# Optimization experiments

Hardware: AMD Instinct MI355X
Metric: run time of the kernel (lower is better)

Reference implementation:

```python
import jax, jax.numpy as jnp
import numpy as np

B, N, C = 2, 65536, 256
H, D, S = 8, 64, 64  # heads, dim_head, slice_num
INNER = H * D


def setup_inputs() -> dict:
    key = jax.random.key(0)
    ks = jax.random.split(key, 8)
    scale_in = 1.0 / np.sqrt(C)
    scale_d = 1.0 / np.sqrt(D)
    return {
        "x": jax.random.normal(ks[0], (B, N, C), dtype=jnp.float32),
        "W_x": jax.random.uniform(ks[1], (C, INNER), jnp.float32, -scale_in, scale_in),
        "b_x": jax.random.uniform(ks[2], (INNER,), jnp.float32, -scale_in, scale_in),
        "W_fx": jax.random.uniform(ks[3], (C, INNER), jnp.float32, -scale_in, scale_in),
        "b_fx": jax.random.uniform(ks[4], (INNER,), jnp.float32, -scale_in, scale_in),
        "W_slice": jax.random.uniform(ks[5], (D, S), jnp.float32, -scale_d, scale_d),
        "b_slice": jax.random.uniform(ks[6], (S,), jnp.float32, -scale_d, scale_d),
        "temperature": jnp.full((1, H, 1, 1), 0.5, dtype=jnp.float32),
    }


def _split_heads(t):
    # (B, N, H*D) -> (B, H, N, D)
    return t.reshape(B, N, H, D).transpose(0, 2, 1, 3)


def reference(x, W_x, b_x, W_fx, b_fx, W_slice, b_slice, temperature):
    projected_x = _split_heads(x @ W_x + b_x)          # (B,H,N,D)
    fx = _split_heads(x @ W_fx + b_fx)                 # (B,H,N,D)
    slice_proj = projected_x @ W_slice + b_slice       # (B,H,N,S)
    temp = jnp.clip(temperature, 0.5, 5.0)
    slice_weights = jax.nn.softmax(slice_proj / temp, axis=-1)  # (B,H,N,S)
    slice_norm = slice_weights.sum(axis=2)             # (B,H,S)
    normed = slice_weights / (slice_norm[:, :, None, :] + 0.01)
    # weighted token aggregation: (B,H,S,D)
    slice_tokens = jnp.einsum("bhns,bhnd->bhsd", normed, fx)
    return slice_tokens
```

## Files before the change

### kernel.cpp

```cpp
#include <hip/hip_runtime.h>

typedef _Float16 f16;
typedef __attribute__((ext_vector_type(8))) _Float16 f16x8;
typedef __attribute__((ext_vector_type(4))) _Float16 f16x4;
typedef __attribute__((ext_vector_type(4))) float    f32x4;

#define MFMA(a,b,c) __builtin_amdgcn_mfma_f32_16x16x32_f16(a,b,c,0,0,0)

constexpr int Bc = 2, Nc = 65536, Cc = 256, Hc = 8;
constexpr int CHUNK = 512;
constexpr int LDX = 72;
constexpr int LDT = 136;


__device__ __forceinline__ f32x4 splat4(float v) { f32x4 r; r.x=v; r.y=v; r.z=v; r.w=v; return r; }
__device__ __forceinline__ f16x8 pack8(float4 a, float4 b) {
  f16x8 r = { (f16)a.x,(f16)a.y,(f16)a.z,(f16)a.w,(f16)b.x,(f16)b.y,(f16)b.z,(f16)b.w };
  return r;
}

__global__ void prep_a(const float* __restrict__ Wx, const float* __restrict__ Wfx,
                       const float* __restrict__ Wsl, const float* __restrict__ bx,
                       const float* __restrict__ bsl, f16* __restrict__ WC,
                       float* __restrict__ bsp) {
  __shared__ float tile[64][72];
  const int b = blockIdx.x, t = threadIdx.x;
  if (b < 32) {
    const int k0 = (b & 3) * 64, c0 = (b >> 2) * 64;
    const int r = t >> 4, c4 = (t & 15) * 4;
    #pragma unroll
    for (int i = 0; i < 4; ++i) {
      float4 v = *(const float4*)&Wfx[(size_t)(k0 + r + i*16)*512 + c0 + c4];
      tile[r + i*16][c4] = v.x; tile[r + i*16][c4+1] = v.y;
      tile[r + i*16][c4+2] = v.z; tile[r + i*16][c4+3] = v.w;
    }
    __syncthreads();
    const int cl = t >> 2, kq = t & 3;
    const int col = c0 + cl, h = col >> 6, n = col & 63;
    f16 tmp[16];
    #pragma unroll
    for (int j = 0; j < 16; ++j) tmp[j] = (f16)tile[kq*16 + j][cl];
    f16* dst = WC + (size_t)(h*128 + n)*256 + k0 + kq*16;
    *(f16x8*)dst       = *(f16x8*)&tmp[0];
    *(f16x8*)(dst + 8) = *(f16x8*)&tmp[8];
  } else if (b < 64) {
    const int k0 = ((b - 32) & 3) * 64, h = (b - 32) >> 2;
    const int k = t & 63, sq = t >> 6;
    float accs[16];
    #pragma unroll
    for (int j = 0; j < 16; ++j) accs[j] = 0.f;
    for (int d = 0; d < 64; ++d) {
      float a = Wx[(size_t)(k0 + k)*512 + h*64 + d];
      #pragma unroll
      for (int j = 0; j < 16; ++j) accs[j] += a * Wsl[d*64 + sq*16 + j];
    }
    #pragma unroll
    for (int j = 0; j < 16; ++j)
      WC[(size_t)(h*128 + 64 + sq*16 + j)*256 + k0 + k] = (f16)accs[j];
  } else {
    for (int u = t; u < 512; u += 256) {
      int h = u >> 6, s = u & 63;
      float a = bsl[s];
      for (int d = 0; d < 64; ++d) a += bx[h*64 + d] * Wsl[d*64 + s];
      bsp[h*64 + s] = a;
    }
  }
}

__global__ __launch_bounds__(256, 2)
void fused_main(const float* __restrict__ x,   const float* __restrict__ bfx,
                const float* __restrict__ bsp, const float* __restrict__ temp,
                const f16* __restrict__ WC,    float* __restrict__ Tg,
                float* __restrict__ normg) {
  __shared__ alignas(16) f16 sm_x  [128 * LDX];
  __shared__ alignas(16) f16 sm_w  [128 * LDX];
  __shared__ alignas(16) f16 sm_fxT[64  * LDT];
  __shared__ alignas(16) f16 sm_wT [64  * LDT];

  const int j    = blockIdx.x;
  const int xcd  = j & 7, slot = j >> 3;
  const int chunk = xcd * 32 + (slot >> 3);
  const int h     = slot & 7;

  const int tid = threadIdx.x;
  const int wv = tid >> 6, lane = tid & 63, quad = lane >> 4, ln = lane & 15;
  const int wm = wv >> 1, wn = wv & 1;
  const long tokBase = (long)chunk * CHUNK;
  const int b  = (int)(tokBase >> 16);
  const int bh = b * Hc + h;

  const float tc = fminf(fmaxf(temp[h], 0.5f), 5.0f);
  const float k2 = 1.44269504f / tc;

  float bv[4];
  {
    const float* bb = (wn == 0) ? (bfx + h*64) : (bsp + h*64);
    #pragma unroll
    for (int nt = 0; nt < 4; ++nt) bv[nt] = bb[nt*16 + ln];
  }

  f32x4 Tacc[2][2];
  #pragma unroll
  for (int i = 0; i < 2; ++i) { Tacc[i][0] = splat4(0.f); Tacc[i][1] = splat4(0.f); }
  float nacc[4] = {0.f, 0.f, 0.f, 0.f};
  const int ci = wv >> 1, cj = wv & 1;

  const f16* WCh = WC + (size_t)h * 128 * 256;

  const int r0 = tid >> 2, seg = tid & 3;
  const int wrow = tid >> 1, whalf = tid & 1;

  float4 xr[8]; f16x8 wr[4];
  auto loadx = [&](int m0, int kb) {
    const float* p = x + (tokBase + (long)m0*128 + r0)*Cc + kb*64 + seg*16;
    xr[0] = *(const float4*)p;        xr[1] = *(const float4*)(p + 4);
    xr[2] = *(const float4*)(p + 8);  xr[3] = *(const float4*)(p + 12);
    p += 64 * Cc;
    xr[4] = *(const float4*)p;        xr[5] = *(const float4*)(p + 4);
    xr[6] = *(const float4*)(p + 8);  xr[7] = *(const float4*)(p + 12);
  };
  auto loadw = [&](int kb) {
    const f16* p = WCh + wrow*256 + kb*64 + whalf*32;
    wr[0] = *(const f16x8*)p;         wr[1] = *(const f16x8*)(p + 8);
    wr[2] = *(const f16x8*)(p + 16);  wr[3] = *(const f16x8*)(p + 24);
  };

  loadx(0, 0); loadw(0);

  for (int m0 = 0; m0 < 4; ++m0) {
    f32x4 acc[4][4];
    #pragma unroll
    for (int mt = 0; mt < 4; ++mt)
      #pragma unroll
      for (int nt = 0; nt < 4; ++nt) acc[mt][nt] = splat4(bv[nt]);

    for (int kb = 0; kb < 4; ++kb) {
      __syncthreads();
      *(f16x8*)&sm_x[r0*LDX + seg*16]          = pack8(xr[0], xr[1]);
      *(f16x8*)&sm_x[r0*LDX + seg*16 + 8]      = pack8(xr[2], xr[3]);
      *(f16x8*)&sm_x[(r0+64)*LDX + seg*16]     = pack8(xr[4], xr[5]);
      *(f16x8*)&sm_x[(r0+64)*LDX + seg*16 + 8] = pack8(xr[6], xr[7]);
      *(f16x8*)&sm_w[wrow*LDX + whalf*32]      = wr[0];
      *(f16x8*)&sm_w[wrow*LDX + whalf*32 +  8] = wr[1];
      *(f16x8*)&sm_w[wrow*LDX + whalf*32 + 16] = wr[2];
      *(f16x8*)&sm_w[wrow*LDX + whalf*32 + 24] = wr[3];
      { int nkb = kb + 1, nm0 = m0;
        if (nkb == 4) { nkb = 0; ++nm0; }
        if (nm0 < 4) { loadx(nm0, nkb); loadw(nkb); } }
      __syncthreads();
      #pragma unroll
      for (int ks = 0; ks < 2; ++ks) {
        f16x8 af[4], bf[4];
        #pragma unroll
        for (int mt = 0; mt < 4; ++mt)
          af[mt] = *(const f16x8*)&sm_x[(wm*64 + mt*16 + ln)*LDX + ks*32 + quad*8];
        #pragma unroll
        for (int nt = 0; nt < 4; ++nt)
          bf[nt] = *(const f16x8*)&sm_w[(wn*64 + nt*16 + ln)*LDX + ks*32 + quad*8];
        #pragma unroll
        for (int mt = 0; mt < 4; ++mt)
          #pragma unroll
          for (int nt = 0; nt < 4; ++nt)
            acc[mt][nt] = MFMA(af[mt], bf[nt], acc[mt][nt]);
      }
    }

    if (wn == 0) {
      #pragma unroll
      for (int mt = 0; mt < 4; ++mt)
        #pragma unroll
        for (int nt = 0; nt < 4; ++nt) {
          f16x4 v = { (f16)acc[mt][nt][0], (f16)acc[mt][nt][1],
                      (f16)acc[mt][nt][2], (f16)acc[mt][nt][3] };
          *(f16x4*)&sm_fxT[(nt*16 + ln)*LDT + wm*64 + mt*16 + quad*4] = v;
        }
    } else {
      #pragma unroll
      for (int mt = 0; mt < 4; ++mt) {
        float wreg[4][4];
        #pragma unroll
        for (int rg = 0; rg < 4; ++rg) {
          float m = fmaxf(fmaxf(acc[mt][0][rg], acc[mt][1][rg]),
                          fmaxf(acc[mt][2][rg], acc[mt][3][rg]));
          #pragma unroll
          for (int dd = 1; dd < 16; dd <<= 1) m = fmaxf(m, __shfl_xor(m, dd, 64));
          float e0 = exp2f((acc[mt][0][rg] - m) * k2);
          float e1 = exp2f((acc[mt][1][rg] - m) * k2);
          float e2 = exp2f((acc[mt][2][rg] - m) * k2);
          float e3 = exp2f((acc[mt][3][rg] - m) * k2);
          float rs = e0 + e1 + e2 + e3;
          #pragma unroll
          for (int dd = 1; dd < 16; dd <<= 1) rs += __shfl_xor(rs, dd, 64);
          float inv = 1.0f / rs;
          wreg[0][rg] = e0*inv; wreg[1][rg] = e1*inv;
          wreg[2][rg] = e2*inv; wreg[3][rg] = e3*inv;
          nacc[0] += wreg[0][rg]; nacc[1] += wreg[1][rg];
          nacc[2] += wreg[2][rg]; nacc[3] += wreg[3][rg];
        }
        #pragma unroll
        for (int nt = 0; nt < 4; ++nt) {
          f16x4 v = { (f16)wreg[nt][0], (f16)wreg[nt][1],
                      (f16)wreg[nt][2], (f16)wreg[nt][3] };
          *(f16x4*)&sm_wT[(nt*16 + ln)*LDT + wm*64 + mt*16 + quad*4] = v;
        }
      }
    }
    __syncthreads();

    #pragma unroll
    for (int ks = 0; ks < 4; ++ks) {
      f16x8 a0 = *(const f16x8*)&sm_wT [(ci*32 +      ln)*LDT + ks*32 + quad*8];
      f16x8 a1 = *(const f16x8*)&sm_wT [(ci*32 + 16 + ln)*LDT + ks*32 + quad*8];
      f16x8 b0 = *(const f16x8*)&sm_fxT[(cj*32 +      ln)*LDT + ks*32 + quad*8];
      f16x8 b1 = *(const f16x8*)&sm_fxT[(cj*32 + 16 + ln)*LDT + ks*32 + quad*8];
      Tacc[0][0] = MFMA(a0, b0, Tacc[0][0]);
      Tacc[0][1] = MFMA(a0, b1, Tacc[0][1]);
      Tacc[1][0] = MFMA(a1, b0, Tacc[1][0]);
      Tacc[1][1] = MFMA(a1, b1, Tacc[1][1]);
    }
  }

  float* Tb = Tg + bh * 4096;
  #pragma unroll
  for (int mt2 = 0; mt2 < 2; ++mt2)
    #pragma unroll
    for (int nt2 = 0; nt2 < 2; ++nt2)
      #pragma unroll
      for (int rg = 0; rg < 4; ++rg) {
        int s = ci*32 + mt2*16 + quad*4 + rg;
        int d = cj*32 + nt2*16 + ln;
        atomicAdd(&Tb[s*64 + d], Tacc[mt2][nt2][rg]);
      }
  if (wn == 1) {
    #pragma unroll
    for (int nt = 0; nt < 4; ++nt) {
      float v = nacc[nt];
      v += __shfl_xor(v, 16, 64);
      v += __shfl_xor(v, 32, 64);
      if (lane < 16) atomicAdd(&normg[bh*64 + nt*16 + ln], v);
    }
  }
}

__global__ void finalize(const float* __restrict__ Tg, const float* __restrict__ normg,
                         float* __restrict__ out) {
  int i = blockIdx.x * 256 + threadIdx.x;
  out[i] = Tg[i] / (normg[i >> 6] + 0.01f);
}

extern "C" void kernel_launch(void* const* d_in, const int* in_sizes, int n_in,
                              void* d_out, int out_size, void* d_ws, size_t ws_size,
                              hipStream_t stream) {
  const float* x    = (const float*)d_in[0];
  const float* Wx   = (const float*)d_in[1];
  const float* bx   = (const float*)d_in[2];
  const float* Wfx  = (const float*)d_in[3];
  const float* bfx  = (const float*)d_in[4];
  const float* Wsl  = (const float*)d_in[5];
  const float* bsl  = (const float*)d_in[6];
  const float* temp = (const float*)d_in[7];
  float* out = (float*)d_out;

  float* Tg    = (float*)d_ws;
  float* normg = Tg + 16 * 4096;
  f16*   WC    = (f16*)((char*)d_ws + 266240);
  float* bsp   = (float*)((char*)d_ws + 790528);

  hipMemsetAsync(d_ws, 0, 266240, stream);
  prep_a    <<<65, 256, 0, stream>>>(Wx, Wfx, Wsl, bx, bsl, WC, bsp);
  fused_main<<<256 * Hc * (CHUNK/512) * 1, 256, 0, stream>>>(x, bfx, bsp, temp, WC, Tg, normg);
  finalize  <<<256, 256, 0, stream>>>(Tg, normg, out);
}
```

Baseline: 368.1 us.

## Alias shared buffers and raise occupancy; drop softmax max subtraction

The transposed fx and weight tiles now reuse the same shared-memory space as the x and W staging tiles, with an extra barrier between the GEMM and the softmax stage. This cuts LDS use per block, and launch bounds are raised to 4 blocks per CU to improve latency hiding. The softmax no longer subtracts the row max, which removes the shuffle-based max reduction but risks exp overflow for large logits. The prep kernel's fused-weight computation is split over more blocks, each doing less work.

```diff
diff --git a/kernel.cpp b/kernel.cpp
--- a/kernel.cpp
+++ b/kernel.cpp
@@ -43,20 +43,21 @@
     f16* dst = WC + (size_t)(h*128 + n)*256 + k0 + kq*16;
     *(f16x8*)dst       = *(f16x8*)&tmp[0];
     *(f16x8*)(dst + 8) = *(f16x8*)&tmp[8];
-  } else if (b < 64) {
-    const int k0 = ((b - 32) & 3) * 64, h = (b - 32) >> 2;
-    const int k = t & 63, sq = t >> 6;
-    float accs[16];
-    #pragma unroll
-    for (int j = 0; j < 16; ++j) accs[j] = 0.f;
+  } else if (b < 96) {
+    const int bb = b - 32;
+    const int h = bb >> 3, k0 = (bb & 7) * 32;
+    const int k = t & 31, sq = t >> 5;
+    float accs[8];
+    #pragma unroll
+    for (int j = 0; j < 8; ++j) accs[j] = 0.f;
     for (int d = 0; d < 64; ++d) {
       float a = Wx[(size_t)(k0 + k)*512 + h*64 + d];
       #pragma unroll
-      for (int j = 0; j < 16; ++j) accs[j] += a * Wsl[d*64 + sq*16 + j];
-    }
-    #pragma unroll
-    for (int j = 0; j < 16; ++j)
-      WC[(size_t)(h*128 + 64 + sq*16 + j)*256 + k0 + k] = (f16)accs[j];
+      for (int j = 0; j < 8; ++j) accs[j] += a * Wsl[d*64 + sq*8 + j];
+    }
+    #pragma unroll
+    for (int j = 0; j < 8; ++j)
+      WC[(size_t)(h*128 + 64 + sq*8 + j)*256 + k0 + k] = (f16)accs[j];
   } else {
     for (int u = t; u < 512; u += 256) {
       int h = u >> 6, s = u & 63;
@@ -67,15 +68,16 @@
   }
 }
 
-__global__ __launch_bounds__(256, 2)
+__global__ __launch_bounds__(256, 4)
 void fused_main(const float* __restrict__ x,   const float* __restrict__ bfx,
                 const float* __restrict__ bsp, const float* __restrict__ temp,
                 const f16* __restrict__ WC,    float* __restrict__ Tg,
                 float* __restrict__ normg) {
-  __shared__ alignas(16) f16 sm_x  [128 * LDX];
-  __shared__ alignas(16) f16 sm_w  [128 * LDX];
-  __shared__ alignas(16) f16 sm_fxT[64  * LDT];
-  __shared__ alignas(16) f16 sm_wT [64  * LDT];
+  __shared__ alignas(16) char smem[2 * 128 * LDX * 2];
+  f16* sm_x   = (f16*)smem;
+  f16* sm_w   = (f16*)(smem + 128*LDX*2);
+  f16* sm_fxT = sm_x;
+  f16* sm_wT  = sm_w;
 
   const int j    = blockIdx.x;
   const int xcd  = j & 7, slot = j >> 3;
@@ -164,6 +166,7 @@
             acc[mt][nt] = MFMA(af[mt], bf[nt], acc[mt][nt]);
       }
     }
+    __syncthreads();
 
     if (wn == 0) {
       #pragma unroll
@@ -177,30 +180,28 @@
     } else {
       #pragma unroll
       for (int mt = 0; mt < 4; ++mt) {
-        float wreg[4][4];
+        float e[4][4], wout[4][4];
+        #pragma unroll
+        for (int nt = 0; nt < 4; ++nt)
+          #pragma unroll
+          for (int rg = 0; rg < 4; ++rg)
+            e[nt][rg] = exp2f(acc[mt][nt][rg] * k2);
         #pragma unroll
         for (int rg = 0; rg < 4; ++rg) {
-          float m = fmaxf(fmaxf(acc[mt][0][rg], acc[mt][1][rg]),
-                          fmaxf(acc[mt][2][rg], acc[mt][3][rg]));
-          #pragma unroll
-          for (int dd = 1; dd < 16; dd <<= 1) m = fmaxf(m, __shfl_xor(m, dd, 64));
-          float e0 = exp2f((acc[mt][0][rg] - m) * k2);
-          float e1 = exp2f((acc[mt][1][rg] - m) * k2);
-          float e2 = exp2f((acc[mt][2][rg] - m) * k2);
-          float e3 = exp2f((acc[mt][3][rg] - m) * k2);
-          float rs = e0 + e1 + e2 + e3;
+          float rs = e[0][rg] + e[1][rg] + e[2][rg] + e[3][rg];
           #pragma unroll
           for (int dd = 1; dd < 16; dd <<= 1) rs += __shfl_xor(rs, dd, 64);
           float inv = 1.0f / rs;
-          wreg[0][rg] = e0*inv; wreg[1][rg] = e1*inv;
-          wreg[2][rg] = e2*inv; wreg[3][rg] = e3*inv;
-          nacc[0] += wreg[0][rg]; nacc[1] += wreg[1][rg];
-          nacc[2] += wreg[2][rg]; nacc[3] += wreg[3][rg];
+          #pragma unroll
+          for (int nt = 0; nt < 4; ++nt) {
+            wout[nt][rg] = e[nt][rg] * inv;
+            nacc[nt] += wout[nt][rg];
+          }
         }
         #pragma unroll
         for (int nt = 0; nt < 4; ++nt) {
-          f16x4 v = { (f16)wreg[nt][0], (f16)wreg[nt][1],
-                      (f16)wreg[nt][2], (f16)wreg[nt][3] };
+          f16x4 v = { (f16)wout[nt][0], (f16)wout[nt][1],
+                      (f16)wout[nt][2], (f16)wout[nt][3] };
           *(f16x4*)&sm_wT[(nt*16 + ln)*LDT + wm*64 + mt*16 + quad*4] = v;
         }
       }
@@ -267,7 +268,7 @@
   float* bsp   = (float*)((char*)d_ws + 790528);
 
   hipMemsetAsync(d_ws, 0, 266240, stream);
-  prep_a    <<<65, 256, 0, stream>>>(Wx, Wfx, Wsl, bx, bsl, WC, bsp);
-  fused_main<<<256 * Hc * (CHUNK/512) * 1, 256, 0, stream>>>(x, bfx, bsp, temp, WC, Tg, normg);
+  prep_a    <<<97, 256, 0, stream>>>(Wx, Wfx, Wsl, bx, bsl, WC, bsp);
+  fused_main<<<2048, 256, 0, stream>>>(x, bfx, bsp, temp, WC, Tg, normg);
   finalize  <<<256, 256, 0, stream>>>(Tg, normg, out);
 }
```

After: 701.0 us. 1.9x slower.
